# Kernel tuning notes

Hardware: AMD Instinct MI355X
Metric: run time of the kernel (lower is better)

The kernel has to match this reference:

```python
import jax, jax.numpy as jnp
import numpy as np
from math import sqrt

BS, SEQ, NV, DM, K = 16, 1024, 512, 256, 8
EPS = 0.05  # sinkhorn epsilon
TEMP = 0.07  # concrete-bernoulli temperature


def setup_inputs() -> dict:
    key = jax.random.key(0)
    k1, k2, k3 = jax.random.split(key, 3)
    x = jax.random.normal(k1, (BS, SEQ, NV), jnp.float32)
    # nn.Linear(seq_len, d_model): weight [d_model, seq_len], bias [d_model]
    W = jax.random.normal(k2, (DM, SEQ), jnp.float32) / sqrt(SEQ)
    b = jnp.zeros((DM,), jnp.float32)
    cluster_emb = jax.random.normal(k3, (K, DM), jnp.float32) / sqrt(DM)
    return {"x": x, "W": W, "b": b, "cluster_emb": cluster_emb}


def _l2norm(z):
    # F.normalize(x, dim=1, p=2) with eps=1e-12 clamp
    n = jnp.maximum(jnp.linalg.norm(z, axis=1, keepdims=True), 1e-12)
    return z / n


def _sinkhorn(q):
    Q = jnp.exp(q / EPS)
    return Q / jnp.sum(Q, axis=1, keepdims=True)


def _concrete_bern(p, key):
    u = jax.random.uniform(key, p.shape, p.dtype, 1e-10, 1.0 - 1e-10)
    noise = jnp.log(u) - jnp.log1p(-u)
    logit = jnp.log(p + 1e-10) - jnp.log(1.0 - p + 1e-10)
    return jax.nn.sigmoid((logit + noise) / TEMP)


def _forward(x, W, b, cluster_emb):
    bs, S, nv = x.shape
    d = W.shape[0]
    k = cluster_emb.shape[0]
    # permute -> [bs, nv, S], Linear(S -> d)
    x_emb = jnp.einsum('bsv,ds->bvd', x, W) + b  # [bs, nv, d]
    x_flat = x_emb.reshape(-1, d)  # [bs*nv, d]
    # cosine-similarity cluster logits
    prob = (_l2norm(x_flat) @ _l2norm(cluster_emb).T).reshape(bs, nv, k)
    prob_temp = _sinkhorn(prob.reshape(-1, k)).reshape(bs, nv, k)  # individual probs
    prob_avg = _sinkhorn(jnp.mean(prob, axis=0))  # [nv, k]
    mask = _concrete_bern(prob_avg, jax.random.key(42))  # [nv, k]
    # CrossAttention with n_heads=1 (dropout inactive in eval)
    scale = 1.0 / sqrt(d)
    scores = jnp.einsum('kd,bvd->bkv', cluster_emb, x_emb)  # [bs, k, nv]
    A = jax.nn.softmax(scale * scores, axis=-1) * mask.T[None]  # masked attn
    V = jnp.einsum('bkv,bvd->bkd', A, x_emb)  # [bs, k, d]
    cluster_emb_avg = jnp.mean(V, axis=0)  # [k, d] (stored attribute in torch)
    # cluster_base_encoding: straight-through bernoulli, broadcast over seq_len
    soft = prob_temp.transpose(2, 0, 1)[..., None]  # [k, bs, nv, 1]
    u = jax.random.uniform(jax.random.key(7), soft.shape, soft.dtype)
    bern = (u < jax.lax.stop_gradient(soft)).astype(soft.dtype)
    extend = jnp.broadcast_to(bern, (k, bs, nv, S))  # [k, bs, nv, S]
    hard = soft + jax.lax.stop_gradient(extend - soft)  # straight-through
    return hard


def reference(x, W, b, cluster_emb):
    return _forward(x, W, b, cluster_emb)
```

## Files before the change

### kernel.cpp

```cpp
#include <hip/hip_runtime.h>
#include <math.h>
#include <stdint.h>

#define BS 16
#define SEQ 1024
#define NV 512
#define DM 256
#define NK 8

__device__ double g_WC[NK * SEQ];
__device__ double g_Bk[NK];
__device__ __align__(16) float g_Wt[SEQ * DM];
__device__ __align__(16) float g_zp[4 * BS * NV * DM];
__device__ double g_nn2[BS * NV];
__device__ double g_Dp[8 * BS * NV * NK];
__device__ unsigned char g_bits[BS * NV];

__device__ __forceinline__ void threefry2x32_key7(uint32_t x0, uint32_t x1,
                                                  uint32_t& o0, uint32_t& o1) {
    const uint32_t k0 = 0u, k1 = 7u;
    const uint32_t k2 = k0 ^ k1 ^ 0x1BD11BDAu;
    uint32_t v0 = x0 + k0, v1 = x1 + k1;
#define TF_ROUND(r) { v0 += v1; v1 = (v1 << (r)) | (v1 >> (32 - (r))); v1 ^= v0; }
    TF_ROUND(13) TF_ROUND(15) TF_ROUND(26) TF_ROUND(6)
    v0 += k1; v1 += k2 + 1u;
    TF_ROUND(17) TF_ROUND(29) TF_ROUND(16) TF_ROUND(24)
    v0 += k2; v1 += k0 + 2u;
    TF_ROUND(13) TF_ROUND(15) TF_ROUND(26) TF_ROUND(6)
    v0 += k0; v1 += k1 + 3u;
    TF_ROUND(17) TF_ROUND(29) TF_ROUND(16) TF_ROUND(24)
    v0 += k1; v1 += k2 + 4u;
    TF_ROUND(13) TF_ROUND(15) TF_ROUND(26) TF_ROUND(6)
    v0 += k2; v1 += k0 + 5u;
#undef TF_ROUND
    o0 = v0; o1 = v1;
}

__device__ __forceinline__ float bits_to_uniform(uint32_t b) {
    return __uint_as_float((b >> 9) | 0x3F800000u) - 1.0f;
}

__global__ __launch_bounds__(256) void prep_merged_kernel(
        const float* __restrict__ W, const float* __restrict__ bias,
        const float* __restrict__ ce) {
    __shared__ float tile[64][132];
    __shared__ double red[256];
    __shared__ double cen[256];
    const int t = threadIdx.x;
    const int bid = blockIdx.x;

    if (bid < 32) {
        const int s0 = (bid & 15) * 64;
        const int d0 = (bid >> 4) * 128;
#pragma unroll
        for (int p = 0; p < 32; ++p) {
            int lin = p * 256 + t;
            int d = lin >> 6, s = lin & 63;
            tile[s][d] = W[(size_t)(d0 + d) * SEQ + s0 + s];
        }
        __syncthreads();
#pragma unroll
        for (int p = 0; p < 32; ++p) {
            int lin = p * 256 + t;
            int s = lin >> 7, d = lin & 127;
            g_Wt[(size_t)(s0 + s) * DM + d0 + d] = tile[s][d];
        }
        return;
    }

    const int pid = bid - 32;
    const int k = pid >> 2;
    const int schunk = pid & 3;

    double c = (double)ce[k * DM + t];
    red[t] = c * c;
    __syncthreads();
    for (int off = 128; off > 0; off >>= 1) {
        if (t < off) red[t] += red[t + off];
        __syncthreads();
    }
    double nc = fmax(sqrt(red[0]), 1e-12);
    cen[t] = c / nc;
    __syncthreads();
    red[t] = (double)bias[t] * cen[t];
    __syncthreads();
    for (int off = 128; off > 0; off >>= 1) {
        if (t < off) red[t] += red[t + off];
        __syncthreads();
    }
    if (t == 0 && schunk == 0) g_Bk[k] = red[0];

    const int s = schunk * 256 + t;
    double acc = 0.0;
#pragma unroll 8
    for (int d = 0; d < DM; ++d)
        acc += cen[d] * (double)W[(size_t)d * SEQ + s];
    g_WC[(size_t)k * SEQ + s] = acc;
}

#define KC 32
#define XS_LD 68
#define WST_LD 264

__global__ __launch_bounds__(256, 2) void gemm_kernel(
        const float* __restrict__ x) {
    __shared__ __align__(16) float xs[KC * XS_LD];
    __shared__ __align__(16) float wst[KC * WST_LD];

    const int t = threadIdx.x;
    const int kblk = blockIdx.x;
    const int vblk = blockIdx.y;
    const int b    = blockIdx.z;
    const int v0 = vblk * 64;
    const float* xb = x + (size_t)b * SEQ * NV;

    const int tv8 = (t & 7) * 8;
    const int grp = t >> 3;
    const int td8 = grp * 8;

    float acc[8][8];
#pragma unroll
    for (int j = 0; j < 8; ++j)
#pragma unroll
        for (int i = 0; i < 8; ++i) acc[j][i] = 0.0f;

    const int sbeg = kblk * 256;
    for (int s0 = sbeg; s0 < sbeg + 256; s0 += KC) {
        __syncthreads();
#pragma unroll
        for (int j = 0; j < 2; ++j) {
            int lin = j * 256 + t;
            int sl = lin >> 4, c4 = (lin & 15) << 2;
            float4 val = *(const float4*)&xb[(size_t)(s0 + sl) * NV + v0 + c4];
            *(float4*)&xs[sl * XS_LD + c4] = val;
        }
#pragma unroll
        for (int j = 0; j < 8; ++j) {
            int lin = j * 256 + t;
            int sl = lin >> 6, c4 = (lin & 63) << 2;
            float4 val = *(const float4*)&g_Wt[(size_t)(s0 + sl) * DM + c4];
            *(float4*)&wst[sl * WST_LD + c4] = val;
        }
        __syncthreads();
#pragma unroll
        for (int kk = 0; kk < KC; ++kk) {
            const float* xr = &xs[kk * XS_LD + tv8];
            const float* wr = &wst[kk * WST_LD + td8];
            float4 xv0 = *(const float4*)(xr);
            float4 xv1 = *(const float4*)(xr + 4);
            float4 wv0 = *(const float4*)(wr);
            float4 wv1 = *(const float4*)(wr + 4);
            float xv[8] = {xv0.x, xv0.y, xv0.z, xv0.w, xv1.x, xv1.y, xv1.z, xv1.w};
            float wv[8] = {wv0.x, wv0.y, wv0.z, wv0.w, wv1.x, wv1.y, wv1.z, wv1.w};
#pragma unroll
            for (int j = 0; j < 8; ++j)
#pragma unroll
                for (int i = 0; i < 8; ++i) acc[j][i] += xv[j] * wv[i];
        }
    }

#pragma unroll
    for (int j = 0; j < 8; ++j) {
        size_t base = (size_t)kblk * (BS * NV * DM) +
                      ((size_t)b * NV + v0 + tv8 + j) * DM + td8;
#pragma unroll
        for (int m = 0; m < 8; m += 4)
            *(float4*)&g_zp[base + m] =
                make_float4(acc[j][m], acc[j][m + 1], acc[j][m + 2], acc[j][m + 3]);
    }
}

__global__ __launch_bounds__(256) void combine_kernel(
        const float* __restrict__ bias) {
    __shared__ double red[16][17];
    const int t = threadIdx.x;
    const int vg = blockIdx.x;
    const int b  = blockIdx.y;
    const int vl = t >> 4, dg = t & 15;
    const int v = vg * 16 + vl;

    const size_t bvbase = ((size_t)b * NV + v) * DM + dg * 16;
    double sq = 0.0;
#pragma unroll
    for (int m = 0; m < 16; m += 4) {
        float4 p0 = *(const float4*)&g_zp[(size_t)0 * (BS * NV * DM) + bvbase + m];
        float4 p1 = *(const float4*)&g_zp[(size_t)1 * (BS * NV * DM) + bvbase + m];
        float4 p2 = *(const float4*)&g_zp[(size_t)2 * (BS * NV * DM) + bvbase + m];
        float4 p3 = *(const float4*)&g_zp[(size_t)3 * (BS * NV * DM) + bvbase + m];
        float4 bb = *(const float4*)&bias[dg * 16 + m];
        double z0 = (double)p0.x + (double)p1.x + (double)p2.x + (double)p3.x + (double)bb.x;
        double z1 = (double)p0.y + (double)p1.y + (double)p2.y + (double)p3.y + (double)bb.y;
        double z2 = (double)p0.z + (double)p1.z + (double)p2.z + (double)p3.z + (double)bb.z;
        double z3 = (double)p0.w + (double)p1.w + (double)p2.w + (double)p3.w + (double)bb.w;
        sq += z0 * z0 + z1 * z1 + z2 * z2 + z3 * z3;
    }
    red[vl][dg] = sq;
    __syncthreads();
    if (dg == 0) {
        double s = 0.0;
#pragma unroll
        for (int i = 0; i < 16; ++i) s += red[vl][i];
        g_nn2[b * NV + v] = s;
    }
}

__global__ __launch_bounds__(256) void dkern(const float* __restrict__ x) {
    __shared__ double wcd[NK][128];
    __shared__ double dw[4][64][NK];
    const int t = threadIdx.x;
    const int vblk = blockIdx.x;
    const int b    = blockIdx.y;
    const int sc   = blockIdx.z;
    const int v0 = vblk * 64;
    const int ss = sc * 128;

#pragma unroll
    for (int j = 0; j < 4; ++j) {
        int idx = j * 256 + t;
        ((double*)wcd)[idx] = g_WC[(size_t)(idx >> 7) * SEQ + ss + (idx & 127)];
    }
    __syncthreads();

    const int vl = t & 63, w = t >> 6;
    const float* xp = x + (size_t)b * SEQ * NV + v0 + vl;
    double D[NK];
#pragma unroll
    for (int k = 0; k < NK; ++k) D[k] = 0.0;
    const int sw = w * 32;
    for (int i = 0; i < 32; ++i) {
        int sl = sw + i;
        double xv = (double)xp[(size_t)(ss + sl) * NV];
#pragma unroll
        for (int k = 0; k < NK; ++k) D[k] += xv * wcd[k][sl];
    }
#pragma unroll
    for (int k = 0; k < NK; ++k) dw[w][vl][k] = D[k];
    __syncthreads();

    const int v = t & 63, k2 = (t >> 6) * 2;
#pragma unroll
    for (int j = 0; j < 2; ++j) {
        int k = k2 + j;
        double s = dw[0][v][k] + dw[1][v][k] + dw[2][v][k] + dw[3][v][k];
        g_Dp[(((size_t)sc * BS + b) * NV + v0 + v) * NK + k] = s;
    }
}

__global__ __launch_bounds__(256) void finalize_kernel() {
    const int bv = blockIdx.x * 256 + threadIdx.x;
    double n = fmax(sqrt(g_nn2[bv]), 1e-12);

    double D[NK];
#pragma unroll
    for (int k = 0; k < NK; ++k) D[k] = g_Bk[k];
#pragma unroll
    for (int sc = 0; sc < 8; ++sc) {
#pragma unroll
        for (int k = 0; k < NK; ++k)
            D[k] += g_Dp[((size_t)sc * (BS * NV) + bv) * NK + k];
    }

    double p[NK], sum = 0.0;
#pragma unroll
    for (int k = 0; k < NK; ++k) {
        p[k] = exp((D[k] / n) / 0.05);
        sum += p[k];
    }
    unsigned int byte = 0;
#pragma unroll
    for (int k = 0; k < NK; ++k) {
        uint32_t i = (uint32_t)(k * (BS * NV) + bv);
        uint32_t y0, y1;
        threefry2x32_key7(0u, i, y0, y1);
        float u = bits_to_uniform(y0 ^ y1);
        if ((double)u < p[k] / sum) byte |= 1u << k;
    }
    g_bits[bv] = (unsigned char)byte;
}

__global__ __launch_bounds__(256) void write_kernel(float* __restrict__ out) {
    const int t = threadIdx.x;
    const size_t r0 = (size_t)blockIdx.x * 8;
#pragma unroll
    for (int j = 0; j < 8; ++j) {
        size_t r = r0 + j;
        unsigned int bv = (unsigned int)(r & 8191u);
        unsigned int k  = (unsigned int)(r >> 13);
        float v = ((g_bits[bv] >> k) & 1u) ? 1.0f : 0.0f;
        float4 val = make_float4(v, v, v, v);
        ((float4*)(out + r * 1024))[t] = val;
    }
}

extern "C" void kernel_launch(void* const* d_in, const int* in_sizes, int n_in,
                              void* d_out, int out_size, void* d_ws, size_t ws_size,
                              hipStream_t stream) {
    const float* x    = (const float*)d_in[0];
    const float* W    = (const float*)d_in[1];
    const float* bias = (const float*)d_in[2];
    const float* ce   = (const float*)d_in[3];
    float* out = (float*)d_out;

    prep_merged_kernel<<<dim3(64), dim3(256), 0, stream>>>(W, bias, ce);
    gemm_kernel<<<dim3(4, 8, 16), dim3(256), 0, stream>>>(x);
    combine_kernel<<<dim3(32, 16), dim3(256), 0, stream>>>(bias);
    dkern<<<dim3(8, 16, 8), dim3(256), 0, stream>>>(x);
    finalize_kernel<<<dim3(32), dim3(256), 0, stream>>>();
    write_kernel<<<dim3(8192), dim3(256), 0, stream>>>(out);
}
```

Before: 387.8 us.

## Double-buffer GEMM tiles with direct global-to-LDS async loads

The x-by-W GEMM kernel now stages its tiles with global_load_lds, copying 16 bytes per lane straight from global memory into LDS without passing through registers. LDS is double-buffered so the next 16-row chunk loads while the current one is computed, and one barrier per chunk replaces two. The K chunk drops from 32 to 16, the padding on the LDS rows is removed (which may add bank conflicts), and the occupancy hint of two blocks per CU is dropped. The direct-to-LDS loads depend on the builtin's per-wave address layout being correct. No explicit wait for those loads is shown, so it relies on the barrier to order them.

```diff
diff --git a/kernel.cpp b/kernel.cpp
--- a/kernel.cpp
+++ b/kernel.cpp
@@ -40,6 +40,13 @@
     return __uint_as_float((b >> 9) | 0x3F800000u) - 1.0f;
 }
 
+__device__ __forceinline__ void cp16(const float* g, float* l) {
+    __builtin_amdgcn_global_load_lds(
+        (const __attribute__((address_space(1))) void*)g,
+        (__attribute__((address_space(3))) void*)l,
+        16, 0, 0);
+}
+
 __global__ __launch_bounds__(256) void prep_merged_kernel(
         const float* __restrict__ W, const float* __restrict__ bias,
         const float* __restrict__ ce) {
@@ -98,25 +105,29 @@
     g_WC[(size_t)k * SEQ + s] = acc;
 }
 
-#define KC 32
-#define XS_LD 68
-#define WST_LD 264
-
-__global__ __launch_bounds__(256, 2) void gemm_kernel(
+#define KC 16
+
+__global__ __launch_bounds__(256) void gemm_kernel(
         const float* __restrict__ x) {
-    __shared__ __align__(16) float xs[KC * XS_LD];
-    __shared__ __align__(16) float wst[KC * WST_LD];
+    __shared__ __align__(16) float xs[2][KC * 64];
+    __shared__ __align__(16) float wst[2][KC * 256];
 
     const int t = threadIdx.x;
     const int kblk = blockIdx.x;
     const int vblk = blockIdx.y;
     const int b    = blockIdx.z;
     const int v0 = vblk * 64;
-    const float* xb = x + (size_t)b * SEQ * NV;
+    const float* xb = x + (size_t)b * SEQ * NV + v0;
 
     const int tv8 = (t & 7) * 8;
-    const int grp = t >> 3;
-    const int td8 = grp * 8;
+    const int td8 = (t >> 3) * 8;
+    const int w = t >> 6;
+    const int l = t & 63;
+
+    const int wrow0 = w * 4;
+    const size_t g_w_lane = (size_t)l * 4;
+    const int xrow_sub = l >> 4;
+    const int xcol = (l & 15) * 4;
 
     float acc[8][8];
 #pragma unroll
@@ -124,28 +135,31 @@
 #pragma unroll
         for (int i = 0; i < 8; ++i) acc[j][i] = 0.0f;
 
+#define STAGE(BUF, S0)                                                         \
+    {                                                                          \
+        _Pragma("unroll")                                                      \
+        for (int j = 0; j < 4; ++j) {                                          \
+            int row = wrow0 + j;                                               \
+            cp16(&g_Wt[(size_t)((S0) + row) * DM + g_w_lane],                  \
+                 &wst[BUF][row * 256]);                                        \
+        }                                                                      \
+        cp16(&xb[(size_t)((S0) + wrow0 + xrow_sub) * NV + xcol],               \
+             &xs[BUF][wrow0 * 64]);                                            \
+    }
+
     const int sbeg = kblk * 256;
-    for (int s0 = sbeg; s0 < sbeg + 256; s0 += KC) {
-        __syncthreads();
-#pragma unroll
-        for (int j = 0; j < 2; ++j) {
-            int lin = j * 256 + t;
-            int sl = lin >> 4, c4 = (lin & 15) << 2;
-            float4 val = *(const float4*)&xb[(size_t)(s0 + sl) * NV + v0 + c4];
-            *(float4*)&xs[sl * XS_LD + c4] = val;
-        }
-#pragma unroll
-        for (int j = 0; j < 8; ++j) {
-            int lin = j * 256 + t;
-            int sl = lin >> 6, c4 = (lin & 63) << 2;
-            float4 val = *(const float4*)&g_Wt[(size_t)(s0 + sl) * DM + c4];
-            *(float4*)&wst[sl * WST_LD + c4] = val;
-        }
-        __syncthreads();
+
+    STAGE(0, sbeg)
+    __syncthreads();
+
+    for (int c = 0; c < 16; ++c) {
+        const int buf = c & 1;
+        if (c < 15) STAGE(buf ^ 1, sbeg + (c + 1) * KC)
+
 #pragma unroll
         for (int kk = 0; kk < KC; ++kk) {
-            const float* xr = &xs[kk * XS_LD + tv8];
-            const float* wr = &wst[kk * WST_LD + td8];
+            const float* xr = &xs[buf][kk * 64 + tv8];
+            const float* wr = &wst[buf][kk * 256 + td8];
             float4 xv0 = *(const float4*)(xr);
             float4 xv1 = *(const float4*)(xr + 4);
             float4 wv0 = *(const float4*)(wr);
@@ -157,7 +171,10 @@
 #pragma unroll
                 for (int i = 0; i < 8; ++i) acc[j][i] += xv[j] * wv[i];
         }
-    }
+
+        __syncthreads();
+    }
+#undef STAGE
 
 #pragma unroll
     for (int j = 0; j < 8; ++j) {
```

Result: no change. 387.0 us (-0.2%).
